# Kernel optimization log

Hardware: AMD Instinct MI355X
Metric: run time of the kernel (lower is better)

Reference implementation:

```python
import jax, jax.numpy as jnp
import numpy as np

N_EMBD = 1024
N_HEAD = 16
HEAD_DIM = N_EMBD // N_HEAD

def setup_inputs() -> dict:
    key = jax.random.key(0)
    ks = jax.random.split(key, 5)
    B, T, C = 2, 2048, N_EMBD
    s = 1.0 / np.sqrt(C)
    x = jax.random.normal(ks[0], (B, T, C), dtype=jnp.float32)
    W_qkv = jax.random.normal(ks[1], (C, 3 * C), dtype=jnp.float32) * s
    b_qkv = jax.random.normal(ks[2], (3 * C,), dtype=jnp.float32) * 0.02
    W_o = jax.random.normal(ks[3], (C, C), dtype=jnp.float32) * s
    b_o = jax.random.normal(ks[4], (C,), dtype=jnp.float32) * 0.02
    return {"x": x, "W_qkv": W_qkv, "b_qkv": b_qkv, "W_o": W_o, "b_o": b_o}

def reference(x, W_qkv, b_qkv, W_o, b_o):
    B, T, C = x.shape
    H, D = N_HEAD, HEAD_DIM
    scale = 1.0 / np.sqrt(D)
    qkv = jnp.einsum('btc,cf->btf', x, W_qkv) + b_qkv  # [B,T,3C]
    q, k, v = jnp.split(qkv, 3, axis=-1)
    # [B,H,T,D]
    q = q.reshape(B, T, H, D).transpose(0, 2, 1, 3)
    k = k.reshape(B, T, H, D).transpose(0, 2, 1, 3)
    v = v.reshape(B, T, H, D).transpose(0, 2, 1, 3)
    att = jnp.einsum('bhqd,bhkd->bhqk', q, k) * scale  # [B,H,T,T]
    causal = jnp.tril(jnp.ones((T, T), dtype=bool))
    att = jnp.where(causal[None, None], att, -jnp.inf)
    att = jax.nn.softmax(att, axis=-1)
    y = jnp.einsum('bhqk,bhkd->bhqd', att, v)  # [B,H,T,D]
    y = y.transpose(0, 2, 1, 3).reshape(B, T, C)
    return jnp.einsum('btc,cf->btf', y, W_o) + b_o
```

## Files before the change

kernel.cpp:

```cpp
#include <hip/hip_runtime.h>
#include <hip/hip_bf16.h>

#define TT 2048
#define BB 2
#define CC 1024
#define NH 16
#define HD 64

typedef __attribute__((ext_vector_type(8))) short short8;
typedef __attribute__((ext_vector_type(4))) short short4b;
typedef __attribute__((ext_vector_type(4))) float f32x4;

typedef unsigned int __attribute__((address_space(1))) ui_gas;
typedef unsigned int __attribute__((address_space(3))) ui_las;

#if __has_builtin(__builtin_amdgcn_mfma_f32_16x16x16bf16_1k)
#define PV16 1
#define VSS 4
#else
#define PV16 0
#define VSS 8
#endif

__device__ __forceinline__ float us2f(unsigned short u) {
    union { unsigned int i; float f; } v; v.i = ((unsigned int)u) << 16; return v.f;
}
__device__ __forceinline__ unsigned short f2us(float f) {
    union { float f; unsigned int i; } v; v.f = f;
    unsigned int i = v.i;
    unsigned int lsb = (i >> 16) & 1u;
    i += 0x7fffu + lsb;
    return (unsigned short)(i >> 16);
}
__device__ __forceinline__ unsigned int pack2_trunc(float a, float b) {
    union { float f; unsigned int u; } x, y; x.f = a; y.f = b;
    return (y.u & 0xffff0000u) | (x.u >> 16);
}

__device__ __forceinline__ void gl_lds16(const unsigned short* g, unsigned short* l) {
    __builtin_amdgcn_global_load_lds((const ui_gas*)g, (ui_las*)l, 16, 0, 0);
}

__device__ __forceinline__ float4 load4(const void* p, size_t i, int isbf) {
    if (isbf) {
        ushort4 u = *reinterpret_cast<const ushort4*>((const unsigned short*)p + i);
        return make_float4(us2f(u.x), us2f(u.y), us2f(u.z), us2f(u.w));
    } else {
        return *reinterpret_cast<const float4*>((const float*)p + i);
    }
}
__device__ __forceinline__ float load1(const void* p, size_t i, int isbf) {
    return isbf ? us2f(((const unsigned short*)p)[i]) : ((const float*)p)[i];
}

__global__ __launch_bounds__(256) void prep_kernel(
    const void* __restrict__ x, const void* __restrict__ Wqkv, const void* __restrict__ Wo,
    const void* __restrict__ bqkv, const void* __restrict__ bo,
    unsigned short* __restrict__ xb, unsigned short* __restrict__ Wqkvt,
    unsigned short* __restrict__ Wot, int* __restrict__ flags)
{
    __shared__ float Ls[64 * 65];
    __shared__ int sh_isbf;
    const int t = threadIdx.x;
    const int bid = blockIdx.x;

    const void* src;
    int mode, sub;
    if (bid < 2048)      { mode = 0; sub = bid;        src = x; }
    else if (bid < 2816) { mode = 1; sub = bid - 2048; src = Wqkv; }
    else                 { mode = 2; sub = bid - 2816; src = Wo; }

    if (bid == 0 && t < 64) {
        const void* ps[5] = {x, Wqkv, bqkv, Wo, bo};
        for (int k = 0; k < 5; ++k) {
            const unsigned short* u = (const unsigned short*)ps[k];
            int bad = 0;
            #pragma unroll
            for (int j = 0; j < 4; ++j) {
                float v = us2f(u[t * 4 + j]);
                if (!(fabsf(v) < 1e4f)) bad = 1;
            }
            unsigned long long m = __ballot(bad != 0);
            if (t == 0) flags[k] = (__popcll(m) < 4) ? 1 : 0;
        }
    }
    if (t < 64) {
        const unsigned short* u = (const unsigned short*)src;
        int bad = 0;
        #pragma unroll
        for (int j = 0; j < 4; ++j) {
            float v = us2f(u[t * 4 + j]);
            if (!(fabsf(v) < 1e4f)) bad = 1;
        }
        unsigned long long m = __ballot(bad != 0);
        if (t == 0) sh_isbf = (__popcll(m) < 4) ? 1 : 0;
    }
    __syncthreads();
    const int isbf = sh_isbf;

    if (mode == 0) {
        const size_t i = ((size_t)sub * 256 + t) * 8;
        float4 a = load4(src, i, isbf);
        float4 b = load4(src, i + 4, isbf);
        alignas(16) unsigned short pk[8];
        pk[0] = f2us(a.x); pk[1] = f2us(a.y); pk[2] = f2us(a.z); pk[3] = f2us(a.w);
        pk[4] = f2us(b.x); pk[5] = f2us(b.y); pk[6] = f2us(b.z); pk[7] = f2us(b.w);
        *reinterpret_cast<uint4*>(xb + i) = *reinterpret_cast<const uint4*>(pk);
        return;
    }

    int N, Krows, n0, k0;
    unsigned short* dst;
    if (mode == 1) { N = 3 * CC; Krows = CC; dst = Wqkvt; n0 = (sub % 48) * 64; k0 = (sub / 48) * 64; }
    else           { N = CC;     Krows = CC; dst = Wot;   n0 = (sub % 16) * 64; k0 = (sub / 16) * 64; }
    {
        const int r = t >> 2, cq = (t & 3) << 4;
        #pragma unroll
        for (int i = 0; i < 4; ++i) {
            float4 v = load4(src, (size_t)(k0 + r) * N + n0 + cq + i * 4, isbf);
            Ls[r * 65 + cq + i * 4 + 0] = v.x;
            Ls[r * 65 + cq + i * 4 + 1] = v.y;
            Ls[r * 65 + cq + i * 4 + 2] = v.z;
            Ls[r * 65 + cq + i * 4 + 3] = v.w;
        }
    }
    __syncthreads();
    {
        const int c = t & 63, kg = (t >> 6) * 16;
        alignas(16) unsigned short pk[16];
        #pragma unroll
        for (int i = 0; i < 16; ++i) pk[i] = f2us(Ls[(kg + i) * 65 + c]);
        unsigned short* d = dst + (size_t)(n0 + c) * Krows + k0 + kg;
        *reinterpret_cast<uint4*>(d + 0) = *reinterpret_cast<const uint4*>(&pk[0]);
        *reinterpret_cast<uint4*>(d + 8) = *reinterpret_cast<const uint4*>(&pk[8]);
    }
}

template<int WM, int WN, int NWM, int NWN>
__global__ __launch_bounds__(256) void gemm_mfma(
    const unsigned short* __restrict__ A,
    const unsigned short* __restrict__ Bt,
    const void* __restrict__ bias, void* __restrict__ C,
    unsigned short* __restrict__ Vt,
    int M, int N, int K,
    const int* __restrict__ flags, int biasfi, int cfi)
{
    constexpr int BM = WM * 16 * NWM, BN = WN * 16 * NWN;
    constexpr int ASL = BM / 16, BSL = BN / 16;

    const int bias_bf = (biasfi >= 0) ? flags[biasfi] : 0;
    const int c_bf    = (cfi >= 0) ? flags[cfi] : ((cfi == -2) ? 1 : 0);

    __shared__ __align__(16) unsigned short Asl[ASL * 2 * 512];
    __shared__ __align__(16) unsigned short Bsl[BSL * 2 * 512];

    const int tid = threadIdx.x;
    const int l  = tid & 63;
    const int w  = tid >> 6;
    const int wm = w / NWN, wn = w % NWN;
    const int bm = blockIdx.y * BM, bn = blockIdx.x * BN;
    const int lm = l & 15;
    const int lk = (l >> 4) * 8;

    f32x4 acc[WM][WN];
    #pragma unroll
    for (int i = 0; i < WM; ++i)
        #pragma unroll
        for (int j = 0; j < WN; ++j) acc[i][j] = (f32x4){0.f, 0.f, 0.f, 0.f};

    for (int k0 = 0; k0 < K; k0 += 64) {
        #pragma unroll
        for (int s = 0; s < ASL / 4; ++s) {
            const int r = w * (ASL / 4) + s;
            #pragma unroll
            for (int kh = 0; kh < 2; ++kh)
                gl_lds16(A + (size_t)(bm + r * 16 + lm) * K + k0 + kh * 32 + lk,
                         &Asl[(r * 2 + kh) * 512]);
        }
        #pragma unroll
        for (int s = 0; s < BSL / 4; ++s) {
            const int r = w * (BSL / 4) + s;
            #pragma unroll
            for (int kh = 0; kh < 2; ++kh)
                gl_lds16(Bt + (size_t)(bn + r * 16 + lm) * K + k0 + kh * 32 + lk,
                         &Bsl[(r * 2 + kh) * 512]);
        }
        __syncthreads();
        #pragma unroll
        for (int kh = 0; kh < 2; ++kh) {
            short8 af[WM], bf[WN];
            #pragma unroll
            for (int i = 0; i < WM; ++i)
                af[i] = *reinterpret_cast<const short8*>(&Asl[((WM * wm + i) * 2 + kh) * 512 + l * 8]);
            #pragma unroll
            for (int j = 0; j < WN; ++j)
                bf[j] = *reinterpret_cast<const short8*>(&Bsl[((WN * wn + j) * 2 + kh) * 512 + l * 8]);
            #pragma unroll
            for (int i = 0; i < WM; ++i)
                #pragma unroll
                for (int j = 0; j < WN; ++j)
                    acc[i][j] = __builtin_amdgcn_mfma_f32_16x16x32_bf16(af[i], bf[j], acc[i][j], 0, 0, 0);
        }
        __syncthreads();
    }

    const int quad = l >> 4;
    float bv[WN];
    #pragma unroll
    for (int j = 0; j < WN; ++j) bv[j] = load1(bias, bn + (WN * wn + j) * 16 + lm, bias_bf);

    #pragma unroll
    for (int i = 0; i < WM; ++i) {
        #pragma unroll
        for (int r = 0; r < 4; ++r) {
            const int row = bm + (WM * wm + i) * 16 + quad * 4 + r;
            #pragma unroll
            for (int j = 0; j < WN; ++j) {
                const int col = bn + (WN * wn + j) * 16 + lm;
                const float val = acc[i][j][r] + bv[j];
                if (c_bf) {
                    const unsigned short us = f2us(val);
                    ((unsigned short*)C)[(size_t)row * N + col] = us;
                    if (Vt != nullptr && col >= 2 * CC) {
                        const int cc2 = col - 2 * CC;
                        const int h = cc2 >> 6, d = cc2 & 63;
                        const int bq = row / TT, tk = row % TT;
                        Vt[((size_t)(bq * NH + h) * HD + d) * TT + tk] = us;
                    }
                } else {
                    ((float*)C)[(size_t)row * N + col] = val;
                }
            }
        }
    }
}

__global__ __launch_bounds__(256) void attn_mfma(
    const unsigned short* __restrict__ qkv,
    const unsigned short* __restrict__ Vt,
    unsigned short* __restrict__ y)
{
    __shared__ __align__(16) unsigned short Ksh[2][8 * 512];
    __shared__ __align__(16) unsigned short Vsh[2][1039 * VSS];

    const int tid = threadIdx.x;
    const int l   = tid & 63;
    const int w   = tid >> 6;
    const int quad = l >> 4;
    const int col  = l & 15;

    const int n  = blockIdx.x;
    const int g  = n >> 3;
    const int bh = (n & 7) * 4 + (g & 3);
    const int i  = g >> 2;
    const int tA = i, tB = 31 - i;
    const int b  = bh >> 4, h = bh & 15;

#if !PV16
    {
        unsigned short* vflat = &Vsh[0][0];
        for (int ss = tid; ss < 1039 * 2; ss += 256)
            *(uint2*)(&vflat[ss * 8 + 4]) = make_uint2(0u, 0u);
    }
#endif

    const float QSCALE = 0.18033688f;
    short8 qfA[2], qfB[2];
    #pragma unroll
    for (int t2 = 0; t2 < 2; ++t2) {
        const int qt = t2 ? tB : tA;
        short8* qf = t2 ? qfB : qfA;
        const int token = qt * 64 + w * 16 + col;
        const unsigned short* qrow = qkv + (size_t)(b * TT + token) * 3 * CC + h * HD;
        #pragma unroll
        for (int ks = 0; ks < 2; ++ks) {
            ushort4 u0 = *(const ushort4*)(qrow + ks * 32 + quad * 8);
            ushort4 u1 = *(const ushort4*)(qrow + ks * 32 + quad * 8 + 4);
            alignas(16) unsigned short pk[8];
            pk[0] = f2us(us2f(u0.x) * QSCALE);
            pk[1] = f2us(us2f(u0.y) * QSCALE);
            pk[2] = f2us(us2f(u0.z) * QSCALE);
            pk[3] = f2us(us2f(u0.w) * QSCALE);
            pk[4] = f2us(us2f(u1.x) * QSCALE);
            pk[5] = f2us(us2f(u1.y) * QSCALE);
            pk[6] = f2us(us2f(u1.z) * QSCALE);
            pk[7] = f2us(us2f(u1.w) * QSCALE);
            qf[ks] = *(const short8*)pk;
        }
    }

    f32x4 oA[4], oB[4];
    #pragma unroll
    for (int nb = 0; nb < 4; ++nb) {
        oA[nb] = (f32x4){0.f, 0.f, 0.f, 0.f};
        oB[nb] = (f32x4){0.f, 0.f, 0.f, 0.f};
    }
    float lAc = 0.f, lBc = 0.f;

    const unsigned short* kbase = qkv + (size_t)b * TT * 3 * CC + CC + h * HD;
    const unsigned short* vbase = Vt + (size_t)bh * HD * TT;

    const int vd = tid >> 2, vg0 = (tid & 3) * 4;

    uint4 rk[2], rv[2];
    auto issue_loads = [&](int kt) {
        const unsigned short* ksrc = kbase + (size_t)(kt * 64 + l) * 3 * CC;
        #pragma unroll
        for (int c2 = 0; c2 < 2; ++c2) {
            const int c = 2 * w + c2;
            rk[c2] = *(const uint4*)(ksrc + c * 8);
        }
        const unsigned short* vsrc = vbase + (size_t)vd * TT + kt * 64 + vg0 * 4;
        rv[0] = *(const uint4*)(vsrc + 0);
        rv[1] = *(const uint4*)(vsrc + 8);
    };
    auto write_lds = [&](int bb) {
        #pragma unroll
        for (int c2 = 0; c2 < 2; ++c2) {
            const int c = 2 * w + c2;
            const int ks = c >> 2, q = c & 3;
            const int slot = ((quad * 2 + ks) * 64 + q * 16 + col) * 8;
            *(uint4*)(&Ksh[bb][slot]) = rk[c2];
        }
        *(uint2*)(&Vsh[bb][((vg0 + 0) * 65 + vd) * VSS]) = make_uint2(rv[0].x, rv[0].y);
        *(uint2*)(&Vsh[bb][((vg0 + 1) * 65 + vd) * VSS]) = make_uint2(rv[0].z, rv[0].w);
        *(uint2*)(&Vsh[bb][((vg0 + 2) * 65 + vd) * VSS]) = make_uint2(rv[1].x, rv[1].y);
        *(uint2*)(&Vsh[bb][((vg0 + 3) * 65 + vd) * VSS]) = make_uint2(rv[1].z, rv[1].w);
    };

    auto step = [&](const short8* qf, f32x4* o, float& l_i, bool diag, int bb) {
        f32x4 st[4];
        #pragma unroll
        for (int nb = 0; nb < 4; ++nb) {
            f32x4 acc = {0.f, 0.f, 0.f, 0.f};
            #pragma unroll
            for (int ks = 0; ks < 2; ++ks) {
                short8 kf = *(const short8*)(&Ksh[bb][((nb * 2 + ks) * 64 + l) * 8]);
                acc = __builtin_amdgcn_mfma_f32_16x16x32_bf16(kf, qf[ks], acc, 0, 0, 0);
            }
            st[nb] = acc;
        }
        float pv[4][4];
        float rs = 0.f;
        #pragma unroll
        for (int nb = 0; nb < 4; ++nb)
            #pragma unroll
            for (int r = 0; r < 4; ++r) {
                float v = st[nb][r];
                if (diag && (nb * 16 + quad * 4 + r > w * 16 + col)) v = -3e38f;
                float p = __builtin_exp2f(v);
                pv[nb][r] = p;
                rs += p;
            }
        rs += __shfl_xor(rs, 16);
        rs += __shfl_xor(rs, 32);
        l_i += rs;
#if PV16
        short4b pf[4];
        #pragma unroll
        for (int nbk = 0; nbk < 4; ++nbk) {
            union { short4b s; unsigned int u[2]; } pk;
            pk.u[0] = pack2_trunc(pv[nbk][0], pv[nbk][1]);
            pk.u[1] = pack2_trunc(pv[nbk][2], pv[nbk][3]);
            pf[nbk] = pk.s;
        }
        #pragma unroll
        for (int nbd = 0; nbd < 4; ++nbd)
            #pragma unroll
            for (int nbk = 0; nbk < 4; ++nbk) {
                short4b vf = *(const short4b*)(&Vsh[bb][((nbk * 4 + quad) * 65 + nbd * 16 + col) * VSS]);
                o[nbd] = __builtin_amdgcn_mfma_f32_16x16x16bf16_1k(pf[nbk], vf, o[nbd], 0, 0, 0);
            }
#else
        short8 pf[4];
        #pragma unroll
        for (int nbk = 0; nbk < 4; ++nbk) {
            union { short8 s; unsigned int u[4]; } pk;
            pk.u[0] = pack2_trunc(pv[nbk][0], pv[nbk][1]);
            pk.u[1] = pack2_trunc(pv[nbk][2], pv[nbk][3]);
            pk.u[2] = 0u; pk.u[3] = 0u;
            pf[nbk] = pk.s;
        }
        #pragma unroll
        for (int nbd = 0; nbd < 4; ++nbd)
            #pragma unroll
            for (int nbk = 0; nbk < 4; ++nbk) {
                short8 vf = *(const short8*)(&Vsh[bb][((nbk * 4 + quad) * 65 + nbd * 16 + col) * VSS]);
                o[nbd] = __builtin_amdgcn_mfma_f32_16x16x32_bf16(pf[nbk], vf, o[nbd], 0, 0, 0);
            }
#endif
    };

    issue_loads(0);
    write_lds(0);
    __syncthreads();
    for (int kt = 0; kt <= tB; ++kt) {
        const int cur = kt & 1;
        if (kt < tB) issue_loads(kt + 1);
        step(qfB, oB, lBc, kt == tB, cur);
        if (kt <= tA) step(qfA, oA, lAc, kt == tA, cur);
        if (kt < tB) write_lds(cur ^ 1);
        __syncthreads();
    }

    #pragma unroll
    for (int t2 = 0; t2 < 2; ++t2) {
        const int qt = t2 ? tB : tA;
        f32x4* o = t2 ? oB : oA;
        const float inv = 1.f / (t2 ? lBc : lAc);
        float invr[4];
        #pragma unroll
        for (int r = 0; r < 4; ++r) invr[r] = __shfl(inv, quad * 4 + r);
        #pragma unroll
        for (int nb = 0; nb < 4; ++nb)
            #pragma unroll
            for (int r = 0; r < 4; ++r) {
                int token = qt * 64 + w * 16 + quad * 4 + r;
                y[(size_t)(b * TT + token) * CC + h * HD + nb * 16 + col] = f2us(o[nb][r] * invr[r]);
            }
    }
}

extern "C" void kernel_launch(void* const* d_in, const int* in_sizes, int n_in,
                              void* d_out, int out_size, void* d_ws, size_t ws_size,
                              hipStream_t stream) {
    const int M = BB * TT;

    char* ws = (char*)d_ws;
    int*            flags = (int*)ws;                         ws += 256;
    unsigned short* xb    = (unsigned short*)ws;              ws += (size_t)M * CC * 2;
    unsigned short* Wqkvt = (unsigned short*)ws;              ws += (size_t)3 * CC * CC * 2;
    unsigned short* Wot   = (unsigned short*)ws;              ws += (size_t)CC * CC * 2;
    unsigned short* qkv   = (unsigned short*)ws;              ws += (size_t)M * 3 * CC * 2;
    unsigned short* Vt    = (unsigned short*)ws;              ws += (size_t)BB * NH * HD * TT * 2;
    unsigned short* y     = (unsigned short*)ws;

    prep_kernel<<<3072, 256, 0, stream>>>(d_in[0], d_in[1], d_in[3], d_in[2], d_in[4],
                                          xb, Wqkvt, Wot, flags);

    gemm_mfma<4, 4, 2, 2><<<dim3(3 * CC / 128, M / 128), 256, 0, stream>>>(
        xb, Wqkvt, d_in[2], qkv, Vt, M, 3 * CC, CC, flags, 2, -2);

    attn_mfma<<<512, 256, 0, stream>>>(qkv, Vt, y);

    gemm_mfma<2, 4, 4, 1><<<dim3(CC / 64, M / 128), 256, 0, stream>>>(
        y, Wot, d_in[4], d_out, nullptr, M, CC, CC, flags, 4, 0);
}
```

Measured before the change: 230.2 us.

## Retile GEMMs, add XCD-aware block swizzle, stage V transpose via LDS, set MFMA priority

Both GEMMs get new tile shapes and launch-bound occupancy hints, plus an XCD-aware block remapping so neighbouring tiles share L2 within each XCD. The scattered per-element V-transpose write in the QKV GEMM epilogue becomes an LDS-staged transpose with 16-byte coalesced stores. The attention kernel raises wave priority around its MFMA sections. The swizzle formulas hardcode grid dimensions (48 and 16), and the extra LDS staging adds a barrier to the epilogue.

```diff
diff --git a/kernel.cpp b/kernel.cpp
--- a/kernel.cpp
+++ b/kernel.cpp
@@ -136,8 +136,8 @@
     }
 }
 
-template<int WM, int WN, int NWM, int NWN>
-__global__ __launch_bounds__(256) void gemm_mfma(
+template<int WM, int WN, int NWM, int NWN, int SWZ, bool VTE, int MINW>
+__global__ __launch_bounds__(256, MINW) void gemm_mfma(
     const unsigned short* __restrict__ A,
     const unsigned short* __restrict__ Bt,
     const void* __restrict__ bias, void* __restrict__ C,
@@ -151,14 +151,30 @@
     const int bias_bf = (biasfi >= 0) ? flags[biasfi] : 0;
     const int c_bf    = (cfi >= 0) ? flags[cfi] : ((cfi == -2) ? 1 : 0);
 
-    __shared__ __align__(16) unsigned short Asl[ASL * 2 * 512];
-    __shared__ __align__(16) unsigned short Bsl[BSL * 2 * 512];
+    __shared__ __align__(16) unsigned short SH[(ASL + BSL) * 2 * 512];
+    unsigned short* Asl = SH;
+    unsigned short* Bsl = SH + ASL * 2 * 512;
 
     const int tid = threadIdx.x;
     const int l  = tid & 63;
     const int w  = tid >> 6;
     const int wm = w / NWN, wn = w % NWN;
-    const int bm = blockIdx.y * BM, bn = blockIdx.x * BN;
+
+    int bx, by;
+    if constexpr (SWZ == 1) {
+        const int lin = blockIdx.y * 48 + blockIdx.x;
+        const int xcd = lin & 7, loc = lin >> 3;
+        bx = (xcd & 3) * 12 + loc % 12;
+        by = (xcd >> 2) * 16 + loc / 12;
+    } else if constexpr (SWZ == 2) {
+        const int lin = blockIdx.y * 16 + blockIdx.x;
+        const int xcd = lin & 7, loc = lin >> 3;
+        bx = (xcd & 1) * 8 + (loc & 7);
+        by = (xcd >> 1) * 16 + (loc >> 3);
+    } else {
+        bx = blockIdx.x; by = blockIdx.y;
+    }
+    const int bm = by * BM, bn = bx * BN;
     const int lm = l & 15;
     const int lk = (l >> 4) * 8;
 
@@ -218,19 +234,39 @@
             for (int j = 0; j < WN; ++j) {
                 const int col = bn + (WN * wn + j) * 16 + lm;
                 const float val = acc[i][j][r] + bv[j];
-                if (c_bf) {
-                    const unsigned short us = f2us(val);
-                    ((unsigned short*)C)[(size_t)row * N + col] = us;
-                    if (Vt != nullptr && col >= 2 * CC) {
-                        const int cc2 = col - 2 * CC;
-                        const int h = cc2 >> 6, d = cc2 & 63;
-                        const int bq = row / TT, tk = row % TT;
-                        Vt[((size_t)(bq * NH + h) * HD + d) * TT + tk] = us;
+                if (c_bf) ((unsigned short*)C)[(size_t)row * N + col] = f2us(val);
+                else      ((float*)C)[(size_t)row * N + col] = val;
+            }
+        }
+    }
+
+    if constexpr (VTE) {
+        constexpr int TS = BM + 8;
+        static_assert(!VTE || BN * TS <= (ASL + BSL) * 2 * 512, "LDS overlay");
+        if (bn >= 2 * CC) {
+            #pragma unroll
+            for (int i = 0; i < WM; ++i)
+                #pragma unroll
+                for (int r = 0; r < 4; ++r) {
+                    const int rl = (WM * wm + i) * 16 + quad * 4 + r;
+                    #pragma unroll
+                    for (int j = 0; j < WN; ++j) {
+                        const int cl2 = (WN * wn + j) * 16 + lm;
+                        SH[cl2 * TS + rl] = f2us(acc[i][j][r] + bv[j]);
                     }
-                } else {
-                    ((float*)C)[(size_t)row * N + col] = val;
                 }
-            }
+            __syncthreads();
+            const int cl = tid >> 2;
+            const int rq = tid & 3;
+            const int cc2 = bn - 2 * CC + cl;
+            const int hh = cc2 >> 6, dd = cc2 & 63;
+            const int bq = bm >> 11;
+            const int tk = (bm & (TT - 1)) + rq * (BM / 4);
+            unsigned short* dst = Vt + ((size_t)(bq * NH + hh) * HD + dd) * TT + tk;
+            const unsigned short* srcp = &SH[cl * TS + rq * (BM / 4)];
+            #pragma unroll
+            for (int k = 0; k < (BM / 4) / 8; ++k)
+                *(uint4*)(dst + k * 8) = *(const uint4*)(srcp + k * 8);
         }
     }
 }
@@ -330,6 +366,7 @@
 
     auto step = [&](const short8* qf, f32x4* o, float& l_i, bool diag, int bb) {
         f32x4 st[4];
+        __builtin_amdgcn_s_setprio(1);
         #pragma unroll
         for (int nb = 0; nb < 4; ++nb) {
             f32x4 acc = {0.f, 0.f, 0.f, 0.f};
@@ -340,6 +377,7 @@
             }
             st[nb] = acc;
         }
+        __builtin_amdgcn_s_setprio(0);
         float pv[4][4];
         float rs = 0.f;
         #pragma unroll
@@ -364,6 +402,7 @@
             pk.u[1] = pack2_trunc(pv[nbk][2], pv[nbk][3]);
             pf[nbk] = pk.s;
         }
+        __builtin_amdgcn_s_setprio(1);
         #pragma unroll
         for (int nbd = 0; nbd < 4; ++nbd)
             #pragma unroll
@@ -371,6 +410,7 @@
                 short4b vf = *(const short4b*)(&Vsh[bb][((nbk * 4 + quad) * 65 + nbd * 16 + col) * VSS]);
                 o[nbd] = __builtin_amdgcn_mfma_f32_16x16x16bf16_1k(pf[nbk], vf, o[nbd], 0, 0, 0);
             }
+        __builtin_amdgcn_s_setprio(0);
 #else
         short8 pf[4];
         #pragma unroll
@@ -381,6 +421,7 @@
             pk.u[2] = 0u; pk.u[3] = 0u;
             pf[nbk] = pk.s;
         }
+        __builtin_amdgcn_s_setprio(1);
         #pragma unroll
         for (int nbd = 0; nbd < 4; ++nbd)
             #pragma unroll
@@ -388,6 +429,7 @@
                 short8 vf = *(const short8*)(&Vsh[bb][((nbk * 4 + quad) * 65 + nbd * 16 + col) * VSS]);
                 o[nbd] = __builtin_amdgcn_mfma_f32_16x16x32_bf16(pf[nbk], vf, o[nbd], 0, 0, 0);
             }
+        __builtin_amdgcn_s_setprio(0);
 #endif
     };
 
@@ -438,11 +480,11 @@
     prep_kernel<<<3072, 256, 0, stream>>>(d_in[0], d_in[1], d_in[3], d_in[2], d_in[4],
                                           xb, Wqkvt, Wot, flags);
 
-    gemm_mfma<4, 4, 2, 2><<<dim3(3 * CC / 128, M / 128), 256, 0, stream>>>(
+    gemm_mfma<2, 4, 4, 1, 1, true, 6><<<dim3(3 * CC / 64, M / 128), 256, 0, stream>>>(
         xb, Wqkvt, d_in[2], qkv, Vt, M, 3 * CC, CC, flags, 2, -2);
 
     attn_mfma<<<512, 256, 0, stream>>>(qkv, Vt, y);
 
-    gemm_mfma<2, 4, 4, 1><<<dim3(CC / 64, M / 128), 256, 0, stream>>>(
+    gemm_mfma<2, 2, 2, 2, 2, false, 4><<<dim3(CC / 64, M / 64), 256, 0, stream>>>(
         y, Wot, d_in[4], d_out, nullptr, M, CC, CC, flags, 4, 0);
 }
```

Measured after the change: 251.2 us. 1.09x slower.
